# Performance work log

Hardware: AMD Instinct MI355X
Metric: run time of the kernel (lower is better)

Reference implementation:

```python
import jax, jax.numpy as jnp
import numpy as np

N_DRUG = 100000
N_PROT = 100000
N_EDGE = 800000
DIM = 128


def _graph_conv(feat_src, esrc, edst, n_src, n_dst, W, b):
    """dgl GraphConv with norm='both': msg = h_src * outdeg^-1/2, sum over in-edges,
    scale by indeg^-1/2, then linear. Degrees clamped to >= 1."""
    ones = jnp.ones(esrc.shape[0], dtype=feat_src.dtype)
    deg_out = jnp.clip(jax.ops.segment_sum(ones, esrc, num_segments=n_src), 1.0)
    deg_in = jnp.clip(jax.ops.segment_sum(ones, edst, num_segments=n_dst), 1.0)
    h = feat_src * jax.lax.rsqrt(deg_out)[:, None]          # [n_src, d]
    agg = jax.ops.segment_sum(h[esrc], edst, num_segments=n_dst)  # [n_dst, d]
    agg = agg * jax.lax.rsqrt(deg_in)[:, None]
    return agg @ W + b


def _hetero_layer(hd, hp, ddi_src, ddi_dst, pdi_src, pdi_dst, ppi_src, ppi_dst, W, b):
    # relation order: 0=DDI (drug->drug), 1=PDI (protein->drug), 2=PPI (protein->protein)
    d_ddi = _graph_conv(hd, ddi_src, ddi_dst, N_DRUG, N_DRUG, W[0], b[0])
    d_pdi = _graph_conv(hp, pdi_src, pdi_dst, N_PROT, N_DRUG, W[1], b[1])
    p_ppi = _graph_conv(hp, ppi_src, ppi_dst, N_PROT, N_PROT, W[2], b[2])
    return d_ddi + d_pdi, p_ppi  # HeteroGraphConv aggregate='sum' per dst type


def setup_inputs() -> dict:
    key = jax.random.key(0)
    ks = jax.random.split(key, 16)
    s = 1.0 / np.sqrt(DIM)
    return {
        "drug_feats": jax.random.normal(ks[0], (N_DRUG, DIM), jnp.float32),
        "protein_feats": jax.random.normal(ks[1], (N_PROT, DIM), jnp.float32),
        "ddi_src": jax.random.randint(ks[2], (N_EDGE,), 0, N_DRUG),
        "ddi_dst": jax.random.randint(ks[3], (N_EDGE,), 0, N_DRUG),
        "pdi_src": jax.random.randint(ks[4], (N_EDGE,), 0, N_PROT),
        "pdi_dst": jax.random.randint(ks[5], (N_EDGE,), 0, N_DRUG),
        "ppi_src": jax.random.randint(ks[6], (N_EDGE,), 0, N_PROT),
        "ppi_dst": jax.random.randint(ks[7], (N_EDGE,), 0, N_PROT),
        "W1": jax.random.normal(ks[8], (3, DIM, DIM), jnp.float32) * s,
        "b1": jnp.zeros((3, DIM), jnp.float32),
        "W2": jax.random.normal(ks[9], (3, DIM, DIM), jnp.float32) * s,
        "b2": jnp.zeros((3, DIM), jnp.float32),
        "W3": jax.random.normal(ks[10], (3, DIM, DIM), jnp.float32) * s,
        "b3": jnp.zeros((3, DIM), jnp.float32),
    }


def reference(drug_feats, protein_feats, ddi_src, ddi_dst, pdi_src, pdi_dst,
              ppi_src, ppi_dst, W1, b1, W2, b2, W3, b3):
    e = (ddi_src, ddi_dst, pdi_src, pdi_dst, ppi_src, ppi_dst)
    hd, hp = _hetero_layer(drug_feats, protein_feats, *e, W1, b1)
    hd, hp = jax.nn.relu(hd), jax.nn.relu(hp)
    hd, hp = _hetero_layer(hd, hp, *e, W2, b2)
    hd, hp = jax.nn.relu(hd), jax.nn.relu(hp)
    hd, hp = _hetero_layer(hd, hp, *e, W3, b3)
    return hd, hp
```

## Files before the change

kernel.cpp:

```cpp
#include <hip/hip_runtime.h>
#include <hip/hip_bf16.h>
#include <stdint.h>

#define NN 100000
#define NE 800000
#define SCAN_CHUNK 2048
#define NBLK 49

#define NPART 8
#define PART_SZ ((NN + NPART - 1) / NPART)
#define KSPLIT 32
#define SEGSZ (NE / KSPLIT)
#define HBINS PART_SZ

typedef __bf16 bf16x8 __attribute__((ext_vector_type(8)));
using float4v = __attribute__((ext_vector_type(4))) float;
typedef int intv4 __attribute__((ext_vector_type(4)));
typedef unsigned short ushortv4 __attribute__((ext_vector_type(4)));

__device__ __forceinline__ float bf2f(unsigned short h) {
    unsigned int u = ((unsigned int)h) << 16;
    return __builtin_bit_cast(float, u);
}
__device__ __forceinline__ float bf_lo(unsigned int u) {
    return __builtin_bit_cast(float, u << 16);
}
__device__ __forceinline__ float bf_hi(unsigned int u) {
    return __builtin_bit_cast(float, u & 0xffff0000u);
}
__device__ __forceinline__ unsigned short f2bf(float x) {
    unsigned int u = __builtin_bit_cast(unsigned int, x);
    u += 0x7fffu + ((u >> 16) & 1u);
    return (unsigned short)(u >> 16);
}

__global__ void detect_fmt(const unsigned short* __restrict__ feat, int* __restrict__ flag) {
    __shared__ int cnt;
    if (threadIdx.x == 0) cnt = 0;
    __syncthreads();
    unsigned int u = feat[threadIdx.x];
    int e = (u >> 7) & 0xFF;
    if (e >= 90 && e <= 143) atomicAdd(&cnt, 1);
    __syncthreads();
    if (threadIdx.x == 0) {
        flag[0] = (cnt >= 160) ? 0 : 1;
        flag[1] = 0;
    }
}

__global__ __launch_bounds__(256) void deg_hist(const int* __restrict__ s0, const int* __restrict__ d0,
                                                const int* __restrict__ s1, const int* __restrict__ d1,
                                                const int* __restrict__ s2, const int* __restrict__ d2,
                                                unsigned short* __restrict__ deg_part) {
    __shared__ unsigned int cnt[HBINS / 2];
    int h = blockIdx.y;
    const int* a;
    switch (h) {
        case 0: a = s0; break;
        case 1: a = s1; break;
        case 2: a = s2; break;
        case 3: a = d0; break;
        case 4: a = d1; break;
        default: a = d2; break;
    }
    int part = blockIdx.x & (NPART - 1);
    int seg = blockIdx.x >> 3;
    int lo = part * HBINS;
    for (int j = threadIdx.x; j < HBINS / 2; j += 256) cnt[j] = 0;
    __syncthreads();
    int base = seg * SEGSZ;
    int end = base + SEGSZ;
    for (int i = base + threadIdx.x * 4; i + 4 <= end; i += 1024) {
        intv4 v = *(const intv4*)(a + i);
#pragma unroll
        for (int k = 0; k < 4; k++) {
            int b = v[k] - lo;
            if ((unsigned)b < (unsigned)HBINS) atomicAdd(&cnt[b >> 1], 1u << ((b & 1) * 16));
        }
    }
    __syncthreads();
    unsigned int* outp = (unsigned int*)(deg_part + (size_t)seg * 6 * NN + (size_t)h * NN + lo);
    for (int j = threadIdx.x; j < HBINS / 2; j += 256) outp[j] = cnt[j];
}

__global__ __launch_bounds__(256) void merge_deg_rs(const unsigned short* __restrict__ deg_part,
                                                    int* __restrict__ deg_all,
                                                    float* __restrict__ rs_all) {
    int i = (blockIdx.x * 256 + threadIdx.x) * 4;
    if (i >= 6 * NN) return;
    int a0 = 0, a1 = 0, a2 = 0, a3 = 0;
#pragma unroll
    for (int s = 0; s < KSPLIT; s++) {
        ushortv4 v = *(const ushortv4*)(deg_part + (size_t)s * 6 * NN + i);
        a0 += v[0]; a1 += v[1]; a2 += v[2]; a3 += v[3];
    }
    intv4 acc; acc[0] = a0; acc[1] = a1; acc[2] = a2; acc[3] = a3;
    *(intv4*)(deg_all + i) = acc;
    float4v r;
#pragma unroll
    for (int k = 0; k < 4; k++) {
        int d = acc[k];
        if (d < 1) d = 1;
        r[k] = rsqrtf((float)d);
    }
    *(float4v*)(rs_all + i) = r;
}

__global__ __launch_bounds__(256) void scan_partial(const int* __restrict__ deg,
                                                    int* __restrict__ bsums) {
    int rel = blockIdx.y, blk = blockIdx.x;
    const int* d = deg + rel * NN;
    int base = blk * SCAN_CHUNK + threadIdx.x * 8;
    int s = 0;
#pragma unroll
    for (int i = 0; i < 8; i++) {
        int idx = base + i;
        if (idx < NN) s += d[idx];
    }
    __shared__ int wsum[4];
#pragma unroll
    for (int off = 32; off; off >>= 1) s += __shfl_down(s, off);
    if ((threadIdx.x & 63) == 0) wsum[threadIdx.x >> 6] = s;
    __syncthreads();
    if (threadIdx.x == 0) bsums[rel * NBLK + blk] = wsum[0] + wsum[1] + wsum[2] + wsum[3];
}

__global__ void scan_bsums(int* bsums) {
    int r = threadIdx.x;
    if (r < 3) {
        int run = 0;
        for (int i = 0; i < NBLK; i++) {
            int t = bsums[r * NBLK + i];
            bsums[r * NBLK + i] = run;
            run += t;
        }
    }
}

__global__ __launch_bounds__(256) void scan_final(const int* __restrict__ deg,
                                                  const int* __restrict__ bsums,
                                                  int* __restrict__ offs) {
    int rel = blockIdx.y, blk = blockIdx.x;
    const int* d = deg + rel * NN;
    int* o = offs + rel * NN;
    int base = blk * SCAN_CHUNK + threadIdx.x * 8;
    int v[8];
    int s = 0;
#pragma unroll
    for (int i = 0; i < 8; i++) {
        int idx = base + i;
        v[i] = (idx < NN) ? d[idx] : 0;
        s += v[i];
    }
    int lane = threadIdx.x & 63, wid = threadIdx.x >> 6;
    int x = s;
#pragma unroll
    for (int off = 1; off < 64; off <<= 1) {
        int t = __shfl_up(x, off);
        if (lane >= off) x += t;
    }
    __shared__ int wsum[4];
    if (lane == 63) wsum[wid] = x;
    __syncthreads();
    int woff = bsums[rel * NBLK + blk];
    for (int i = 0; i < wid; i++) woff += wsum[i];
    int run = woff + x - s;
#pragma unroll
    for (int i = 0; i < 8; i++) {
        int idx = base + i;
        if (idx < NN) {
            o[idx] = run;
            run += v[i];
        }
    }
}

__global__ __launch_bounds__(256) void seg_start_k(const unsigned short* __restrict__ deg_part,
                                                   const int* __restrict__ offs_all,
                                                   int* __restrict__ seg_start) {
    int i = blockIdx.x * 256 + threadIdx.x;
    if (i >= 3 * NN) return;
    int rel = i / NN, node = i - rel * NN;
    int run = offs_all[i];
#pragma unroll
    for (int s = 0; s < KSPLIT; s++) {
        seg_start[((size_t)s * 3 + rel) * NN + node] = run;
        run += deg_part[((size_t)s * 6 + 3 + rel) * NN + node];
    }
}

__global__ __launch_bounds__(256) void csr_fill3s(const int* __restrict__ s0, const int* __restrict__ d0,
                                                  const int* __restrict__ s1, const int* __restrict__ d1,
                                                  const int* __restrict__ s2, const int* __restrict__ d2,
                                                  const int* __restrict__ seg_start,
                                                  int* __restrict__ csr_all) {
    __shared__ int cur[PART_SZ];
    int rel = blockIdx.y;
    const int* s = (rel == 0) ? s0 : ((rel == 1) ? s1 : s2);
    const int* d = (rel == 0) ? d0 : ((rel == 1) ? d1 : d2);
    int part = blockIdx.x & (NPART - 1);
    int seg = blockIdx.x >> 3;
    int lo = part * PART_SZ;
    const int* ss = seg_start + ((size_t)seg * 3 + rel) * NN + lo;
    for (int j = threadIdx.x; j < PART_SZ; j += 256) cur[j] = ss[j];
    __syncthreads();
    int* csr = csr_all + (size_t)rel * NE;
    int base = seg * SEGSZ;
    int end = base + SEGSZ;
    for (int i = base + threadIdx.x * 4; i + 4 <= end; i += 1024) {
        intv4 dv = *(const intv4*)(d + i);
        intv4 sv = *(const intv4*)(s + i);
#pragma unroll
        for (int k = 0; k < 4; k++) {
            int b = dv[k] - lo;
            if ((unsigned)b < (unsigned)PART_SZ) {
                int pos = atomicAdd(&cur[b], 1);
                csr[pos] = sv[k];
            }
        }
    }
}

__global__ __launch_bounds__(256) void swizzle_w9(const void* __restrict__ W0,
                                                  const void* __restrict__ W1,
                                                  const void* __restrict__ W2,
                                                  unsigned short* __restrict__ Wf,
                                                  const int* __restrict__ fmtp) {
    int yy = blockIdx.y;
    int l = yy / 3, rel = yy - l * 3;
    const void* W = (l == 0) ? W0 : ((l == 1) ? W1 : W2);
    int fmt = fmtp[0];
    int idx = blockIdx.x * 256 + threadIdx.x;
    if (idx >= 16384) return;
    int j = idx & 7, lane = (idx >> 3) & 63, nt = (idx >> 9) & 7, ks = idx >> 12;
    int k = ks * 32 + (lane >> 4) * 8 + j;
    int n = nt * 16 + (lane & 15);
    int e = rel * 16384 + k * 128 + n;
    Wf[(size_t)yy * 16384 + idx] = fmt ? f2bf(((const float*)W)[e]) : ((const unsigned short*)W)[e];
}

__global__ void bias_prep3(const void* __restrict__ b0, const void* __restrict__ b1,
                           const void* __restrict__ b2, float* __restrict__ bd,
                           float* __restrict__ bp, const int* __restrict__ fmtp) {
    int l = blockIdx.x;
    const void* b = (l == 0) ? b0 : ((l == 1) ? b1 : b2);
    int fmt = fmtp[0];
    int n = threadIdx.x;
    float v0, v1, v2;
    if (fmt) {
        const float* bf = (const float*)b;
        v0 = bf[n]; v1 = bf[128 + n]; v2 = bf[256 + n];
    } else {
        const unsigned short* bh = (const unsigned short*)b;
        v0 = bf2f(bh[n]); v1 = bf2f(bh[128 + n]); v2 = bf2f(bh[256 + n]);
    }
    bd[l * 128 + n] = v0 + v1;
    bp[l * 128 + n] = v2;
}

__global__ __launch_bounds__(256) void gemmT(const void* __restrict__ Ad,
                                             const void* __restrict__ Ap,
                                             const unsigned short* __restrict__ Wf,
                                             unsigned short* __restrict__ T0,
                                             unsigned short* __restrict__ T1,
                                             unsigned short* __restrict__ T2,
                                             const int* __restrict__ ifmtp) {
    int y = blockIdx.y;
    int ifmt = ifmtp[0];
    const void* A = y ? Ap : Ad;
    int lid = threadIdx.x & 63, wid = threadIdx.x >> 6;
    int m0 = blockIdx.x * 64 + wid * 16;
    int ra = m0 + (lid & 15);
    if (ra > NN - 1) ra = NN - 1;
    int koff = (lid >> 4) * 8;
    bf16x8 a[4];
    if (ifmt) {
        const float* Af = (const float*)A + (size_t)ra * 128 + koff;
#pragma unroll
        for (int ks = 0; ks < 4; ks++) {
            float4 u = *(const float4*)(Af + ks * 32);
            float4 v = *(const float4*)(Af + ks * 32 + 4);
            union { bf16x8 b; unsigned short s[8]; } t;
            t.s[0] = f2bf(u.x); t.s[1] = f2bf(u.y); t.s[2] = f2bf(u.z); t.s[3] = f2bf(u.w);
            t.s[4] = f2bf(v.x); t.s[5] = f2bf(v.y); t.s[6] = f2bf(v.z); t.s[7] = f2bf(v.w);
            a[ks] = t.b;
        }
    } else {
        const unsigned short* Ah = (const unsigned short*)A + (size_t)ra * 128 + koff;
#pragma unroll
        for (int ks = 0; ks < 4; ks++) a[ks] = *(const bf16x8*)(Ah + ks * 32);
    }
    int nouts = y ? 2 : 1;
    for (int o = 0; o < nouts; o++) {
        int rel = y ? (1 + o) : 0;
        const bf16x8* bb = (const bf16x8*)(Wf + (size_t)rel * 16384);
        float4v acc[8];
#pragma unroll
        for (int nt = 0; nt < 8; nt++) acc[nt] = (float4v){0.f, 0.f, 0.f, 0.f};
#pragma unroll
        for (int ks = 0; ks < 4; ks++) {
#pragma unroll
            for (int nt = 0; nt < 8; nt++) {
                bf16x8 b = bb[ks * 512 + nt * 64 + lid];
                acc[nt] = __builtin_amdgcn_mfma_f32_16x16x32_bf16(a[ks], b, acc[nt], 0, 0, 0);
            }
        }
        unsigned short* T = (rel == 0) ? T0 : ((rel == 1) ? T1 : T2);
        int crow = m0 + (lid >> 4) * 4;
        int ccol = lid & 15;
#pragma unroll
        for (int nt = 0; nt < 8; nt++) {
#pragma unroll
            for (int r = 0; r < 4; r++) {
                int row = crow + r;
                if (row < NN) T[(size_t)row * 128 + nt * 16 + ccol] = f2bf(acc[nt][r]);
            }
        }
    }
}

__device__ __forceinline__ void acc8v(float* acc, uint4 v, float w) {
    acc[0] = fmaf(bf_lo(v.x), w, acc[0]);
    acc[1] = fmaf(bf_hi(v.x), w, acc[1]);
    acc[2] = fmaf(bf_lo(v.y), w, acc[2]);
    acc[3] = fmaf(bf_hi(v.y), w, acc[3]);
    acc[4] = fmaf(bf_lo(v.z), w, acc[4]);
    acc[5] = fmaf(bf_hi(v.z), w, acc[5]);
    acc[6] = fmaf(bf_lo(v.w), w, acc[6]);
    acc[7] = fmaf(bf_hi(v.w), w, acc[7]);
}

__device__ __forceinline__ void gather8(const unsigned short* __restrict__ T,
                                        const float* __restrict__ rs_out,
                                        const int* __restrict__ cp, int cnt, int lane,
                                        float* acc) {
    int e = 0;
    for (; e + 4 <= cnt; e += 4) {
        int i0 = cp[e], i1 = cp[e + 1], i2 = cp[e + 2], i3 = cp[e + 3];
        float w0 = rs_out[i0], w1 = rs_out[i1], w2 = rs_out[i2], w3 = rs_out[i3];
        uint4 v0 = *(const uint4*)(T + (size_t)i0 * 128 + lane * 8);
        uint4 v1 = *(const uint4*)(T + (size_t)i1 * 128 + lane * 8);
        uint4 v2 = *(const uint4*)(T + (size_t)i2 * 128 + lane * 8);
        uint4 v3 = *(const uint4*)(T + (size_t)i3 * 128 + lane * 8);
        acc8v(acc, v0, w0);
        acc8v(acc, v1, w1);
        acc8v(acc, v2, w2);
        acc8v(acc, v3, w3);
    }
    for (; e < cnt; e++) {
        int i0 = cp[e];
        float w0 = rs_out[i0];
        uint4 v0 = *(const uint4*)(T + (size_t)i0 * 128 + lane * 8);
        acc8v(acc, v0, w0);
    }
}

__global__ __launch_bounds__(256) void agg_out(const unsigned short* __restrict__ T0,
                                               const unsigned short* __restrict__ T1,
                                               const unsigned short* __restrict__ T2,
                                               const float* __restrict__ rs_all,
                                               const int* __restrict__ offs_all,
                                               const int* __restrict__ deg_in_all,
                                               const int* __restrict__ csr_all,
                                               const float* __restrict__ bdl,
                                               const float* __restrict__ bpl,
                                               void* __restrict__ outv,
                                               int relu, const int* __restrict__ ofmt) {
    int y = blockIdx.y;
    int g = blockIdx.x * 256 + threadIdx.x;
    int dst = g >> 4;
    int lane = g & 15;
    if (dst >= NN) return;
    int fmt = ofmt[0];
    float out8[8] = {0.f, 0.f, 0.f, 0.f, 0.f, 0.f, 0.f, 0.f};
    const float* bias;
    int row;
    if (y == 0) {
        {
            const int* cp = csr_all + offs_all[dst];
            int cnt = deg_in_all[dst];
            float acc[8] = {0.f, 0.f, 0.f, 0.f, 0.f, 0.f, 0.f, 0.f};
            gather8(T0, rs_all, cp, cnt, lane, acc);
            float si = rs_all[3 * NN + dst];
#pragma unroll
            for (int j = 0; j < 8; j++) out8[j] = fmaf(si, acc[j], out8[j]);
        }
        {
            const int* cp = csr_all + NE + offs_all[NN + dst];
            int cnt = deg_in_all[NN + dst];
            float acc[8] = {0.f, 0.f, 0.f, 0.f, 0.f, 0.f, 0.f, 0.f};
            gather8(T1, rs_all + NN, cp, cnt, lane, acc);
            float si = rs_all[4 * NN + dst];
#pragma unroll
            for (int j = 0; j < 8; j++) out8[j] = fmaf(si, acc[j], out8[j]);
        }
        bias = bdl;
        row = dst;
    } else {
        const int* cp = csr_all + 2 * NE + offs_all[2 * NN + dst];
        int cnt = deg_in_all[2 * NN + dst];
        float acc[8] = {0.f, 0.f, 0.f, 0.f, 0.f, 0.f, 0.f, 0.f};
        gather8(T2, rs_all + 2 * NN, cp, cnt, lane, acc);
        float si = rs_all[5 * NN + dst];
#pragma unroll
        for (int j = 0; j < 8; j++) out8[j] = si * acc[j];
        bias = bpl;
        row = NN + dst;
    }
    float v[8];
#pragma unroll
    for (int j = 0; j < 8; j++) {
        float t = out8[j] + bias[lane * 8 + j];
        v[j] = relu ? fmaxf(t, 0.f) : t;
    }
    size_t base = (size_t)row * 128 + lane * 8;
    if (fmt) {
        float* o = (float*)outv + base;
        float4 u0; u0.x = v[0]; u0.y = v[1]; u0.z = v[2]; u0.w = v[3];
        float4 u1; u1.x = v[4]; u1.y = v[5]; u1.z = v[6]; u1.w = v[7];
        *(float4*)o = u0;
        *(float4*)(o + 4) = u1;
    } else {
        unsigned short* o = (unsigned short*)outv + base;
        uint4 u;
        u.x = (unsigned int)f2bf(v[0]) | ((unsigned int)f2bf(v[1]) << 16);
        u.y = (unsigned int)f2bf(v[2]) | ((unsigned int)f2bf(v[3]) << 16);
        u.z = (unsigned int)f2bf(v[4]) | ((unsigned int)f2bf(v[5]) << 16);
        u.w = (unsigned int)f2bf(v[6]) | ((unsigned int)f2bf(v[7]) << 16);
        *(uint4*)o = u;
    }
}

extern "C" void kernel_launch(void* const* d_in, const int* in_sizes, int n_in,
                              void* d_out, int out_size, void* d_ws, size_t ws_size,
                              hipStream_t stream) {
    (void)in_sizes; (void)n_in; (void)out_size;
    const void* drug = d_in[0];
    const void* prot = d_in[1];
    const int* ddi_src = (const int*)d_in[2];
    const int* ddi_dst = (const int*)d_in[3];
    const int* pdi_src = (const int*)d_in[4];
    const int* pdi_dst = (const int*)d_in[5];
    const int* ppi_src = (const int*)d_in[6];
    const int* ppi_dst = (const int*)d_in[7];
    const void* Wl[3] = {d_in[8], d_in[10], d_in[12]};
    const void* bl[3] = {d_in[9], d_in[11], d_in[13]};

    char* p = (char*)d_ws;
    auto alloc = [&](size_t bytes) -> char* {
        char* r = p;
        p += (bytes + 255) & ~(size_t)255;
        return r;
    };
    int*   flag       = (int*)alloc(256);
    int*   deg_all    = (int*)alloc(6 * NN * 4);
    float* rs_all     = (float*)alloc(6 * NN * 4);
    int*   offs_all   = (int*)alloc(3 * NN * 4);
    int*   csr_all    = (int*)alloc(3 * NE * 4);
    int*   bsums      = (int*)alloc(3 * NBLK * 4);
    int*   seg_start  = (int*)alloc((size_t)KSPLIT * 3 * NN * 4);
    char*  hbuf       = alloc((size_t)NN * 128 * 4);
    unsigned short* hbuf_lo = (unsigned short*)hbuf;
    unsigned short* hbuf_hi = (unsigned short*)hbuf + (size_t)NN * 128;
    unsigned short* Wf = (unsigned short*)alloc(9 * 16384 * 2);
    float* bd = (float*)alloc(3 * 128 * 4);
    float* bp = (float*)alloc(3 * 128 * 4);
    size_t needed = (size_t)(p - (char*)d_ws);
    if (needed > ws_size) return;

    unsigned short* deg_part = (unsigned short*)hbuf;
    unsigned short* Tws = (unsigned short*)seg_start;

    const int* FMT = flag;
    const int* BF  = flag + 1;

    unsigned short* dout_lo = (unsigned short*)d_out;
    unsigned short* dout_hi = (unsigned short*)d_out + (size_t)NN * 128;

    detect_fmt<<<1, 256, 0, stream>>>((const unsigned short*)drug, flag);

    deg_hist<<<dim3(NPART * KSPLIT, 6), 256, 0, stream>>>(ddi_src, ddi_dst, pdi_src, pdi_dst,
                                                          ppi_src, ppi_dst, deg_part);
    merge_deg_rs<<<(6 * NN / 4 + 255) / 256, 256, 0, stream>>>(deg_part, deg_all, rs_all);
    scan_partial<<<dim3(NBLK, 3), 256, 0, stream>>>(deg_all + 3 * NN, bsums);
    scan_bsums<<<1, 64, 0, stream>>>(bsums);
    scan_final<<<dim3(NBLK, 3), 256, 0, stream>>>(deg_all + 3 * NN, bsums, offs_all);
    seg_start_k<<<(3 * NN + 255) / 256, 256, 0, stream>>>(deg_part, offs_all, seg_start);
    csr_fill3s<<<dim3(NPART * KSPLIT, 3), 256, 0, stream>>>(ddi_src, ddi_dst, pdi_src, pdi_dst,
                                                            ppi_src, ppi_dst, seg_start, csr_all);

    swizzle_w9<<<dim3(64, 9), 256, 0, stream>>>(Wl[0], Wl[1], Wl[2], Wf, FMT);
    bias_prep3<<<3, 128, 0, stream>>>(bl[0], bl[1], bl[2], bd, bp, FMT);

    const int TGB = (NN + 63) / 64;
    const int AGB = (NN * 16) / 256;
    gemmT<<<dim3(TGB, 2), 256, 0, stream>>>(drug, prot, Wf, hbuf_lo, hbuf_hi, Tws, FMT);
    agg_out<<<dim3(AGB, 2), 256, 0, stream>>>(hbuf_lo, hbuf_hi, Tws, rs_all, offs_all,
                                              deg_all + 3 * NN, csr_all, bd, bp,
                                              d_out, 1, BF);
    gemmT<<<dim3(TGB, 2), 256, 0, stream>>>(dout_lo, dout_hi, Wf + 3 * 16384,
                                            dout_lo, dout_hi, Tws, BF);
    agg_out<<<dim3(AGB, 2), 256, 0, stream>>>(dout_lo, dout_hi, Tws, rs_all, offs_all,
                                              deg_all + 3 * NN, csr_all, bd + 128, bp + 128,
                                              hbuf, 1, BF);
    gemmT<<<dim3(TGB, 2), 256, 0, stream>>>(hbuf_lo, hbuf_hi, Wf + 6 * 16384,
                                            hbuf_lo, hbuf_hi, Tws, BF);
    agg_out<<<dim3(AGB, 2), 256, 0, stream>>>(hbuf_lo, hbuf_hi, Tws, rs_all, offs_all,
                                              deg_all + 3 * NN, csr_all, bd + 2 * 128, bp + 2 * 128,
                                              d_out, 0, FMT);
}
```

Baseline: 697.0 us.

## Fuse degree/scan/segment-start kernels and fold source-degree scaling into GEMM epilogue

Merges the degree merge, partial scan, bsum scan, final scan and segment-start kernels into two kernels. Each scan block now sums the preceding block totals itself, and the weight swizzle and bias prep run as one launch. The out-degree rsqrt scaling moves from the per-edge gather into the GEMM epilogue, so aggregation no longer does a random rs_out load per edge, and the gather unroll goes from 4 to 8 edges. The costs are fewer blocks for the merge and seg_start work, which may reduce parallelism, and rounding to bf16 after the scaling instead of before it.

```diff
diff --git a/kernel.cpp b/kernel.cpp
--- a/kernel.cpp
+++ b/kernel.cpp
@@ -83,41 +83,54 @@
     for (int j = threadIdx.x; j < HBINS / 2; j += 256) outp[j] = cnt[j];
 }
 
-__global__ __launch_bounds__(256) void merge_deg_rs(const unsigned short* __restrict__ deg_part,
-                                                    int* __restrict__ deg_all,
-                                                    float* __restrict__ rs_all) {
-    int i = (blockIdx.x * 256 + threadIdx.x) * 4;
-    if (i >= 6 * NN) return;
-    int a0 = 0, a1 = 0, a2 = 0, a3 = 0;
-#pragma unroll
-    for (int s = 0; s < KSPLIT; s++) {
-        ushortv4 v = *(const ushortv4*)(deg_part + (size_t)s * 6 * NN + i);
-        a0 += v[0]; a1 += v[1]; a2 += v[2]; a3 += v[3];
-    }
-    intv4 acc; acc[0] = a0; acc[1] = a1; acc[2] = a2; acc[3] = a3;
-    *(intv4*)(deg_all + i) = acc;
-    float4v r;
-#pragma unroll
-    for (int k = 0; k < 4; k++) {
-        int d = acc[k];
-        if (d < 1) d = 1;
-        r[k] = rsqrtf((float)d);
-    }
-    *(float4v*)(rs_all + i) = r;
-}
-
-__global__ __launch_bounds__(256) void scan_partial(const int* __restrict__ deg,
-                                                    int* __restrict__ bsums) {
+__global__ __launch_bounds__(256) void merge_scan(const unsigned short* __restrict__ deg_part,
+                                                  int* __restrict__ deg_all,
+                                                  float* __restrict__ rs_all,
+                                                  int* __restrict__ bsums) {
     int rel = blockIdx.y, blk = blockIdx.x;
-    const int* d = deg + rel * NN;
-    int base = blk * SCAN_CHUNK + threadIdx.x * 8;
-    int s = 0;
-#pragma unroll
-    for (int i = 0; i < 8; i++) {
-        int idx = base + i;
-        if (idx < NN) s += d[idx];
+    int node0 = blk * SCAN_CHUNK + threadIdx.x * 8;
+    int chunk_sum = 0;
+#pragma unroll
+    for (int reg = 0; reg < 2; reg++) {
+        int eoff = (reg ? (3 + rel) : rel) * NN;
+#pragma unroll
+        for (int half = 0; half < 2; half++) {
+            int n = node0 + half * 4;
+            if (n + 4 <= NN) {
+                int a0 = 0, a1 = 0, a2 = 0, a3 = 0;
+                for (int s = 0; s < KSPLIT; s++) {
+                    ushortv4 v = *(const ushortv4*)(deg_part + (size_t)s * 6 * NN + eoff + n);
+                    a0 += v[0]; a1 += v[1]; a2 += v[2]; a3 += v[3];
+                }
+                intv4 acc; acc[0] = a0; acc[1] = a1; acc[2] = a2; acc[3] = a3;
+                *(intv4*)(deg_all + eoff + n) = acc;
+                float4v r;
+#pragma unroll
+                for (int k = 0; k < 4; k++) {
+                    int d = acc[k];
+                    if (d < 1) d = 1;
+                    r[k] = rsqrtf((float)d);
+                }
+                *(float4v*)(rs_all + eoff + n) = r;
+                if (reg) chunk_sum += a0 + a1 + a2 + a3;
+            } else {
+                for (int j = 0; j < 4; j++) {
+                    int nn = n + j;
+                    if (nn < NN) {
+                        int a = 0;
+                        for (int s = 0; s < KSPLIT; s++)
+                            a += deg_part[(size_t)s * 6 * NN + eoff + nn];
+                        deg_all[eoff + nn] = a;
+                        int d = a < 1 ? 1 : a;
+                        rs_all[eoff + nn] = rsqrtf((float)d);
+                        if (reg) chunk_sum += a;
+                    }
+                }
+            }
+        }
     }
     __shared__ int wsum[4];
+    int s = chunk_sum;
 #pragma unroll
     for (int off = 32; off; off >>= 1) s += __shfl_down(s, off);
     if ((threadIdx.x & 63) == 0) wsum[threadIdx.x >> 6] = s;
@@ -125,21 +138,11 @@
     if (threadIdx.x == 0) bsums[rel * NBLK + blk] = wsum[0] + wsum[1] + wsum[2] + wsum[3];
 }
 
-__global__ void scan_bsums(int* bsums) {
-    int r = threadIdx.x;
-    if (r < 3) {
-        int run = 0;
-        for (int i = 0; i < NBLK; i++) {
-            int t = bsums[r * NBLK + i];
-            bsums[r * NBLK + i] = run;
-            run += t;
-        }
-    }
-}
-
-__global__ __launch_bounds__(256) void scan_final(const int* __restrict__ deg,
-                                                  const int* __restrict__ bsums,
-                                                  int* __restrict__ offs) {
+__global__ __launch_bounds__(256) void scan_seg(const int* __restrict__ deg,
+                                                const int* __restrict__ bsums,
+                                                const unsigned short* __restrict__ deg_part,
+                                                int* __restrict__ offs,
+                                                int* __restrict__ seg_start) {
     int rel = blockIdx.y, blk = blockIdx.x;
     const int* d = deg + rel * NN;
     int* o = offs + rel * NN;
@@ -162,30 +165,30 @@
     __shared__ int wsum[4];
     if (lane == 63) wsum[wid] = x;
     __syncthreads();
-    int woff = bsums[rel * NBLK + blk];
+    int woff = 0;
+    for (int i = 0; i < blk; i++) woff += bsums[rel * NBLK + i];
     for (int i = 0; i < wid; i++) woff += wsum[i];
     int run = woff + x - s;
+    int runs[8];
+#pragma unroll
+    for (int i = 0; i < 8; i++) {
+        int idx = base + i;
+        runs[i] = run;
+        if (idx < NN) {
+            o[idx] = run;
+            run += v[i];
+        }
+    }
 #pragma unroll
     for (int i = 0; i < 8; i++) {
         int idx = base + i;
         if (idx < NN) {
-            o[idx] = run;
-            run += v[i];
-        }
-    }
-}
-
-__global__ __launch_bounds__(256) void seg_start_k(const unsigned short* __restrict__ deg_part,
-                                                   const int* __restrict__ offs_all,
-                                                   int* __restrict__ seg_start) {
-    int i = blockIdx.x * 256 + threadIdx.x;
-    if (i >= 3 * NN) return;
-    int rel = i / NN, node = i - rel * NN;
-    int run = offs_all[i];
-#pragma unroll
-    for (int s = 0; s < KSPLIT; s++) {
-        seg_start[((size_t)s * 3 + rel) * NN + node] = run;
-        run += deg_part[((size_t)s * 6 + 3 + rel) * NN + node];
+            int r2 = runs[i];
+            for (int sg = 0; sg < KSPLIT; sg++) {
+                seg_start[((size_t)sg * 3 + rel) * NN + idx] = r2;
+                r2 += deg_part[((size_t)sg * 6 + 3 + rel) * NN + idx];
+            }
+        }
     }
 }
 
@@ -221,15 +224,38 @@
     }
 }
 
-__global__ __launch_bounds__(256) void swizzle_w9(const void* __restrict__ W0,
-                                                  const void* __restrict__ W1,
-                                                  const void* __restrict__ W2,
-                                                  unsigned short* __restrict__ Wf,
-                                                  const int* __restrict__ fmtp) {
+__global__ __launch_bounds__(256) void prep_wb(const void* __restrict__ W0,
+                                               const void* __restrict__ W1,
+                                               const void* __restrict__ W2,
+                                               const void* __restrict__ b0,
+                                               const void* __restrict__ b1,
+                                               const void* __restrict__ b2,
+                                               unsigned short* __restrict__ Wf,
+                                               float* __restrict__ bd, float* __restrict__ bp,
+                                               const int* __restrict__ fmtp) {
     int yy = blockIdx.y;
+    int fmt = fmtp[0];
+    if (yy == 9) {
+        if (blockIdx.x == 0 && threadIdx.x < 128) {
+            int n = threadIdx.x;
+            for (int l = 0; l < 3; l++) {
+                const void* b = (l == 0) ? b0 : ((l == 1) ? b1 : b2);
+                float v0, v1, v2;
+                if (fmt) {
+                    const float* bf = (const float*)b;
+                    v0 = bf[n]; v1 = bf[128 + n]; v2 = bf[256 + n];
+                } else {
+                    const unsigned short* bh = (const unsigned short*)b;
+                    v0 = bf2f(bh[n]); v1 = bf2f(bh[128 + n]); v2 = bf2f(bh[256 + n]);
+                }
+                bd[l * 128 + n] = v0 + v1;
+                bp[l * 128 + n] = v2;
+            }
+        }
+        return;
+    }
     int l = yy / 3, rel = yy - l * 3;
     const void* W = (l == 0) ? W0 : ((l == 1) ? W1 : W2);
-    int fmt = fmtp[0];
     int idx = blockIdx.x * 256 + threadIdx.x;
     if (idx >= 16384) return;
     int j = idx & 7, lane = (idx >> 3) & 63, nt = (idx >> 9) & 7, ks = idx >> 12;
@@ -239,28 +265,10 @@
     Wf[(size_t)yy * 16384 + idx] = fmt ? f2bf(((const float*)W)[e]) : ((const unsigned short*)W)[e];
 }
 
-__global__ void bias_prep3(const void* __restrict__ b0, const void* __restrict__ b1,
-                           const void* __restrict__ b2, float* __restrict__ bd,
-                           float* __restrict__ bp, const int* __restrict__ fmtp) {
-    int l = blockIdx.x;
-    const void* b = (l == 0) ? b0 : ((l == 1) ? b1 : b2);
-    int fmt = fmtp[0];
-    int n = threadIdx.x;
-    float v0, v1, v2;
-    if (fmt) {
-        const float* bf = (const float*)b;
-        v0 = bf[n]; v1 = bf[128 + n]; v2 = bf[256 + n];
-    } else {
-        const unsigned short* bh = (const unsigned short*)b;
-        v0 = bf2f(bh[n]); v1 = bf2f(bh[128 + n]); v2 = bf2f(bh[256 + n]);
-    }
-    bd[l * 128 + n] = v0 + v1;
-    bp[l * 128 + n] = v2;
-}
-
 __global__ __launch_bounds__(256) void gemmT(const void* __restrict__ Ad,
                                              const void* __restrict__ Ap,
                                              const unsigned short* __restrict__ Wf,
+                                             const float* __restrict__ rs_all,
                                              unsigned short* __restrict__ T0,
                                              unsigned short* __restrict__ T1,
                                              unsigned short* __restrict__ T2,
@@ -290,6 +298,8 @@
 #pragma unroll
         for (int ks = 0; ks < 4; ks++) a[ks] = *(const bf16x8*)(Ah + ks * 32);
     }
+    int crow = m0 + (lid >> 4) * 4;
+    int ccol = lid & 15;
     int nouts = y ? 2 : 1;
     for (int o = 0; o < nouts; o++) {
         int rel = y ? (1 + o) : 0;
@@ -305,53 +315,53 @@
                 acc[nt] = __builtin_amdgcn_mfma_f32_16x16x32_bf16(a[ks], b, acc[nt], 0, 0, 0);
             }
         }
+        float rs_o[4];
+#pragma unroll
+        for (int r = 0; r < 4; r++) {
+            int rr = crow + r;
+            if (rr > NN - 1) rr = NN - 1;
+            rs_o[r] = rs_all[rel * NN + rr];
+        }
         unsigned short* T = (rel == 0) ? T0 : ((rel == 1) ? T1 : T2);
-        int crow = m0 + (lid >> 4) * 4;
-        int ccol = lid & 15;
 #pragma unroll
         for (int nt = 0; nt < 8; nt++) {
 #pragma unroll
             for (int r = 0; r < 4; r++) {
                 int row = crow + r;
-                if (row < NN) T[(size_t)row * 128 + nt * 16 + ccol] = f2bf(acc[nt][r]);
+                if (row < NN) T[(size_t)row * 128 + nt * 16 + ccol] = f2bf(acc[nt][r] * rs_o[r]);
             }
         }
     }
 }
 
-__device__ __forceinline__ void acc8v(float* acc, uint4 v, float w) {
-    acc[0] = fmaf(bf_lo(v.x), w, acc[0]);
-    acc[1] = fmaf(bf_hi(v.x), w, acc[1]);
-    acc[2] = fmaf(bf_lo(v.y), w, acc[2]);
-    acc[3] = fmaf(bf_hi(v.y), w, acc[3]);
-    acc[4] = fmaf(bf_lo(v.z), w, acc[4]);
-    acc[5] = fmaf(bf_hi(v.z), w, acc[5]);
-    acc[6] = fmaf(bf_lo(v.w), w, acc[6]);
-    acc[7] = fmaf(bf_hi(v.w), w, acc[7]);
-}
-
-__device__ __forceinline__ void gather8(const unsigned short* __restrict__ T,
-                                        const float* __restrict__ rs_out,
+__device__ __forceinline__ void accT(float* acc, uint4 v) {
+    acc[0] += bf_lo(v.x); acc[1] += bf_hi(v.x);
+    acc[2] += bf_lo(v.y); acc[3] += bf_hi(v.y);
+    acc[4] += bf_lo(v.z); acc[5] += bf_hi(v.z);
+    acc[6] += bf_lo(v.w); acc[7] += bf_hi(v.w);
+}
+
+__device__ __forceinline__ void gatherT(const unsigned short* __restrict__ T,
                                         const int* __restrict__ cp, int cnt, int lane,
                                         float* acc) {
     int e = 0;
-    for (; e + 4 <= cnt; e += 4) {
+    for (; e + 8 <= cnt; e += 8) {
         int i0 = cp[e], i1 = cp[e + 1], i2 = cp[e + 2], i3 = cp[e + 3];
-        float w0 = rs_out[i0], w1 = rs_out[i1], w2 = rs_out[i2], w3 = rs_out[i3];
+        int i4 = cp[e + 4], i5 = cp[e + 5], i6 = cp[e + 6], i7 = cp[e + 7];
         uint4 v0 = *(const uint4*)(T + (size_t)i0 * 128 + lane * 8);
         uint4 v1 = *(const uint4*)(T + (size_t)i1 * 128 + lane * 8);
         uint4 v2 = *(const uint4*)(T + (size_t)i2 * 128 + lane * 8);
         uint4 v3 = *(const uint4*)(T + (size_t)i3 * 128 + lane * 8);
-        acc8v(acc, v0, w0);
-        acc8v(acc, v1, w1);
-        acc8v(acc, v2, w2);
-        acc8v(acc, v3, w3);
+        uint4 v4 = *(const uint4*)(T + (size_t)i4 * 128 + lane * 8);
+        uint4 v5 = *(const uint4*)(T + (size_t)i5 * 128 + lane * 8);
+        uint4 v6 = *(const uint4*)(T + (size_t)i6 * 128 + lane * 8);
+        uint4 v7 = *(const uint4*)(T + (size_t)i7 * 128 + lane * 8);
+        accT(acc, v0); accT(acc, v1); accT(acc, v2); accT(acc, v3);
+        accT(acc, v4); accT(acc, v5); accT(acc, v6); accT(acc, v7);
     }
     for (; e < cnt; e++) {
-        int i0 = cp[e];
-        float w0 = rs_out[i0];
-        uint4 v0 = *(const uint4*)(T + (size_t)i0 * 128 + lane * 8);
-        acc8v(acc, v0, w0);
+        uint4 v0 = *(const uint4*)(T + (size_t)cp[e] * 128 + lane * 8);
+        accT(acc, v0);
     }
 }
 
@@ -380,7 +390,7 @@
             const int* cp = csr_all + offs_all[dst];
             int cnt = deg_in_all[dst];
             float acc[8] = {0.f, 0.f, 0.f, 0.f, 0.f, 0.f, 0.f, 0.f};
-            gather8(T0, rs_all, cp, cnt, lane, acc);
+            gatherT(T0, cp, cnt, lane, acc);
             float si = rs_all[3 * NN + dst];
 #pragma unroll
             for (int j = 0; j < 8; j++) out8[j] = fmaf(si, acc[j], out8[j]);
@@ -389,7 +399,7 @@
             const int* cp = csr_all + NE + offs_all[NN + dst];
             int cnt = deg_in_all[NN + dst];
             float acc[8] = {0.f, 0.f, 0.f, 0.f, 0.f, 0.f, 0.f, 0.f};
-            gather8(T1, rs_all + NN, cp, cnt, lane, acc);
+            gatherT(T1, cp, cnt, lane, acc);
             float si = rs_all[4 * NN + dst];
 #pragma unroll
             for (int j = 0; j < 8; j++) out8[j] = fmaf(si, acc[j], out8[j]);
@@ -400,7 +410,7 @@
         const int* cp = csr_all + 2 * NE + offs_all[2 * NN + dst];
         int cnt = deg_in_all[2 * NN + dst];
         float acc[8] = {0.f, 0.f, 0.f, 0.f, 0.f, 0.f, 0.f, 0.f};
-        gather8(T2, rs_all + 2 * NN, cp, cnt, lane, acc);
+        gatherT(T2, cp, cnt, lane, acc);
         float si = rs_all[5 * NN + dst];
 #pragma unroll
         for (int j = 0; j < 8; j++) out8[j] = si * acc[j];
@@ -481,29 +491,27 @@
 
     deg_hist<<<dim3(NPART * KSPLIT, 6), 256, 0, stream>>>(ddi_src, ddi_dst, pdi_src, pdi_dst,
                                                           ppi_src, ppi_dst, deg_part);
-    merge_deg_rs<<<(6 * NN / 4 + 255) / 256, 256, 0, stream>>>(deg_part, deg_all, rs_all);
-    scan_partial<<<dim3(NBLK, 3), 256, 0, stream>>>(deg_all + 3 * NN, bsums);
-    scan_bsums<<<1, 64, 0, stream>>>(bsums);
-    scan_final<<<dim3(NBLK, 3), 256, 0, stream>>>(deg_all + 3 * NN, bsums, offs_all);
-    seg_start_k<<<(3 * NN + 255) / 256, 256, 0, stream>>>(deg_part, offs_all, seg_start);
+    merge_scan<<<dim3(NBLK, 3), 256, 0, stream>>>(deg_part, deg_all, rs_all, bsums);
+    scan_seg<<<dim3(NBLK, 3), 256, 0, stream>>>(deg_all + 3 * NN, bsums, deg_part,
+                                                offs_all, seg_start);
     csr_fill3s<<<dim3(NPART * KSPLIT, 3), 256, 0, stream>>>(ddi_src, ddi_dst, pdi_src, pdi_dst,
                                                             ppi_src, ppi_dst, seg_start, csr_all);
 
-    swizzle_w9<<<dim3(64, 9), 256, 0, stream>>>(Wl[0], Wl[1], Wl[2], Wf, FMT);
-    bias_prep3<<<3, 128, 0, stream>>>(bl[0], bl[1], bl[2], bd, bp, FMT);
+    prep_wb<<<dim3(64, 10), 256, 0, stream>>>(Wl[0], Wl[1], Wl[2], bl[0], bl[1], bl[2],
+                                              Wf, bd, bp, FMT);
 
     const int TGB = (NN + 63) / 64;
     const int AGB = (NN * 16) / 256;
-    gemmT<<<dim3(TGB, 2), 256, 0, stream>>>(drug, prot, Wf, hbuf_lo, hbuf_hi, Tws, FMT);
+    gemmT<<<dim3(TGB, 2), 256, 0, stream>>>(drug, prot, Wf, rs_all, hbuf_lo, hbuf_hi, Tws, FMT);
     agg_out<<<dim3(AGB, 2), 256, 0, stream>>>(hbuf_lo, hbuf_hi, Tws, rs_all, offs_all,
                                               deg_all + 3 * NN, csr_all, bd, bp,
                                               d_out, 1, BF);
-    gemmT<<<dim3(TGB, 2), 256, 0, stream>>>(dout_lo, dout_hi, Wf + 3 * 16384,
+    gemmT<<<dim3(TGB, 2), 256, 0, stream>>>(dout_lo, dout_hi, Wf + 3 * 16384, rs_all,
                                             dout_lo, dout_hi, Tws, BF);
     agg_out<<<dim3(AGB, 2), 256, 0, stream>>>(dout_lo, dout_hi, Tws, rs_all, offs_all,
                                               deg_all + 3 * NN, csr_all, bd + 128, bp + 128,
                                               hbuf, 1, BF);
-    gemmT<<<dim3(TGB, 2), 256, 0, stream>>>(hbuf_lo, hbuf_hi, Wf + 6 * 16384,
+    gemmT<<<dim3(TGB, 2), 256, 0, stream>>>(hbuf_lo, hbuf_hi, Wf + 6 * 16384, rs_all,
                                             hbuf_lo, hbuf_hi, Tws, BF);
     agg_out<<<dim3(AGB, 2), 256, 0, stream>>>(hbuf_lo, hbuf_hi, Tws, rs_all, offs_all,
                                               deg_all + 3 * NN, csr_all, bd + 2 * 128, bp + 2 * 128,
```

Result: slower. 822.9 us (+18.1%).
